# Performance work log

Hardware: AMD Instinct MI355X
Metric: run time of the kernel (lower is better)

The kernel has to match this reference:

```python
import jax, jax.numpy as jnp
import numpy as np

B, S, L, D, M = 32, 256, 64, 100, 20  # batch, n_sentences, max_sentence_len, embed_dim, n_memories


def setup_inputs() -> dict:
    key = jax.random.key(0)
    ks = jax.random.split(key, 6)
    batch = jax.random.normal(ks[0], (B, S, L, D), dtype=jnp.float32)
    enc_mult = jnp.ones((L, D), dtype=jnp.float32)  # input_encoder_multiplier (init to ones)
    keys = 0.1 * jax.random.normal(ks[1], (M, D), dtype=jnp.float32)
    U = 0.1 * jax.random.normal(ks[2], (D, D), dtype=jnp.float32)  # nn.Linear weight [out,in]
    V = 0.1 * jax.random.normal(ks[3], (D, D), dtype=jnp.float32)
    W = 0.1 * jax.random.normal(ks[4], (D, D), dtype=jnp.float32)
    prelu_a = jnp.ones((), dtype=jnp.float32)  # PReLU(init=1), single shared parameter
    return {"batch": batch, "enc_mult": enc_mult, "keys": keys, "U": U, "V": V, "W": W, "prelu_a": prelu_a}


def reference(batch, enc_mult, keys, U, V, W, prelu_a):
    # Encode: elementwise multiply by learned positional multiplier, sum over words -> [B, S, D]
    enc = (batch * enc_mult).sum(axis=2)

    def prelu(x):
        return jnp.where(x >= 0, x, prelu_a * x)

    # keys @ V.T is step-invariant
    keysV = jnp.einsum('md,ed->me', keys, V)  # [M, D]

    def step(mem, s):  # mem: [B, M, D], s: [B, D]
        memory_gate = jnp.einsum('bd,bmd->bm', s, mem)          # [B, M]
        key_gate = jnp.einsum('bd,md->bm', s, keys)              # [B, M]
        gate = jax.nn.sigmoid(memory_gate + key_gate)            # [B, M]
        cand = prelu(
            jnp.einsum('bmd,ed->bme', mem, U)                    # U(memories)
            + keysV[None, :, :]                                  # V(keys)
            + jnp.einsum('bd,ed->be', s, W)[:, None, :]          # W(sentence), broadcast over M
        )
        mem = mem + cand * gate[:, :, None]
        mem = mem / jnp.linalg.norm(mem, axis=2, keepdims=True)  # L2 normalize each memory slot
        return mem, None

    mem0 = jnp.broadcast_to(keys[None, :, :], (B, M, D))  # memories init = keys repeated per batch
    mem_final, _ = jax.lax.scan(step, mem0, jnp.swapaxes(enc, 0, 1))  # scan over sentences
    return mem_final
```

## Files before the change

### kernel.cpp

```cpp
#include <hip/hip_runtime.h>


typedef float v2f __attribute__((ext_vector_type(2)));

__global__ __launch_bounds__(320) void encode_k(
    const float* __restrict__ batch,
    const float* __restrict__ encm,
    float* __restrict__ enc)
{
    __shared__ float prod[6400];
    __shared__ float part[200];
    const int t = threadIdx.x;
    const int row = blockIdx.x;
    const float4* rb = (const float4*)batch + (size_t)row * 1600;
    const float4* e4 = (const float4*)encm;
    float4* p4 = (float4*)prod;
    #pragma unroll
    for (int i = 0; i < 5; ++i) {
        const int idx = i * 320 + t;
        float4 x = rb[idx];
        float4 mu = e4[idx];
        float4 p;
        p.x = x.x * mu.x; p.y = x.y * mu.y; p.z = x.z * mu.z; p.w = x.w * mu.w;
        p4[idx] = p;
    }
    __syncthreads();
    if (t < 200) {
        const int c = (t < 100) ? t : (t - 100);
        const int l0 = (t < 100) ? 0 : 32;
        float s0 = 0.f, s1 = 0.f;
        #pragma unroll
        for (int l = 0; l < 32; l += 2) {
            s0 += prod[(l0 + l) * 100 + c];
            s1 += prod[(l0 + l + 1) * 100 + c];
        }
        part[t] = s0 + s1;
    }
    __syncthreads();
    if (t < 100) enc[(size_t)row * 100 + t] = part[t] + part[100 + t];
}

__global__ void prep_k(const float* __restrict__ W,
                       const float* __restrict__ keys,
                       float* __restrict__ T)
{
    const int d = blockIdx.x;
    const int e = threadIdx.x;
    float v = 0.f;
    if (e < 100) v = W[e * 100 + d];
    else if (e < 120) v = keys[(e - 100) * 100 + d];
    T[d * 128 + e] = v;
}

__global__ __launch_bounds__(128) void project_k(
    const float* __restrict__ enc,
    const float* __restrict__ T,
    float* __restrict__ sWp,
    float* __restrict__ kg)
{
    __shared__ float encS[400];
    const int t = threadIdx.x;
    const int row0 = blockIdx.x * 4;
    if (t < 100) ((float4*)encS)[t] = ((const float4*)(enc + (size_t)row0 * 100))[t];
    __syncthreads();
    float a0 = 0.f, a1 = 0.f, a2 = 0.f, a3 = 0.f;
    #pragma unroll 4
    for (int d = 0; d < 100; ++d) {
        const float w = T[d * 128 + t];
        a0 += w * encS[d];
        a1 += w * encS[100 + d];
        a2 += w * encS[200 + d];
        a3 += w * encS[300 + d];
    }
    if (t < 100) {
        sWp[(size_t)row0 * 100 + t]       = a0;
        sWp[(size_t)(row0 + 1) * 100 + t] = a1;
        sWp[(size_t)(row0 + 2) * 100 + t] = a2;
        sWp[(size_t)(row0 + 3) * 100 + t] = a3;
    } else if (t < 120) {
        const int m = t - 100;
        kg[(size_t)row0 * 20 + m]       = a0;
        kg[(size_t)(row0 + 1) * 20 + m] = a1;
        kg[(size_t)(row0 + 2) * 20 + m] = a2;
        kg[(size_t)(row0 + 3) * 20 + m] = a3;
    }
}

template <int CTRL>
__device__ __forceinline__ float dpp_add_f(float x) {
    int s = __builtin_amdgcn_update_dpp(0, __float_as_int(x), CTRL, 0xF, 0xF, true);
    return x + __int_as_float(s);
}
#define DPP6(v) v = dpp_add_f<0x111>(v); v = dpp_add_f<0x112>(v); v = dpp_add_f<0x114>(v); \
                v = dpp_add_f<0x118>(v); v = dpp_add_f<0x142>(v); v = dpp_add_f<0x143>(v);

#define MATVEC(QOUT, CBPTR)                                             \
    {                                                                   \
        v2f A0 = {0.f,0.f}, A1 = {0.f,0.f};                             \
        v2f A2 = {0.f,0.f}, A3 = {0.f,0.f};                             \
        _Pragma("unroll")                                               \
        for (int j = 0; j < 25; ++j) {                                  \
            float4 cc = (CBPTR)[j];                                     \
            v2f lo = {cc.x, cc.y}, hi4 = {cc.z, cc.w};                  \
            if (j & 1) {                                                \
                A2 = __builtin_elementwise_fma(UE[2*j],   lo,  A2);     \
                A3 = __builtin_elementwise_fma(UE[2*j+1], hi4, A3);     \
            } else {                                                    \
                A0 = __builtin_elementwise_fma(UE[2*j],   lo,  A0);     \
                A1 = __builtin_elementwise_fma(UE[2*j+1], hi4, A1);     \
            }                                                           \
        }                                                               \
        v2f S = (A0 + A1) + (A2 + A3);                                  \
        QOUT = S.x + S.y;                                               \
    }

__global__ __launch_bounds__(128) void entnet_scan(
    const float* __restrict__ enc,
    const float* __restrict__ sWp,
    const float* __restrict__ kg,
    const float* __restrict__ keys,
    const float* __restrict__ U,
    const float* __restrict__ V,
    const float* __restrict__ paPtr,
    float* __restrict__ out)
{
    __shared__ float4 cbuf4[2][32];
    __shared__ float4 red[2][2];
    float* cbuf = (float*)cbuf4;
    const int tid  = threadIdx.x;
    const int lane = tid & 63;
    const int wid  = tid >> 6;
    const int xcd = blockIdx.x & 7;
    const int gg  = blockIdx.x >> 3;
    const int b = xcd * 4 + gg / 20;
    const int m = gg % 20;
    const bool act = (tid < 100);
    const float h = act ? 1.f : 0.f;
    const int e = act ? tid : 99;
    const float pa = paPtr[0];

    v2f UE[50];
    {
        const float4* u = (const float4*)(U + e * 100);
        #pragma unroll
        for (int k = 0; k < 25; ++k) {
            float4 a = u[k];
            UE[2*k]   = (v2f){a.x, a.y};
            UE[2*k+1] = (v2f){a.z, a.w};
        }
    }

    float kv = 0.f;
    {
        const float4* km = (const float4*)(keys + m * 100);
        const float4* vv = (const float4*)(V + e * 100);
        #pragma unroll
        for (int k = 0; k < 25; ++k) {
            float4 a = vv[k], kk = km[k];
            kv += a.x * kk.x + a.y * kk.y + a.z * kk.z + a.w * kk.w;
        }
    }

    const float* encRow = enc + (size_t)b * 25600;
    const float* sWRow  = sWp + (size_t)b * 25600;
    const float* kgRow  = kg + (size_t)b * 5120 + m;

    const float k0 = keys[m * 100 + e];
    float nm = k0;

    cbuf[128 + tid] = k0;
    float nq  = h * k0 * k0;
    const float sv0 = encRow[e];
    float q1i = h * sv0 * k0;
    DPP6(nq) DPP6(q1i)
    if (lane == 63) red[1][wid] = (float4){nq, q1i, 0.f, 0.f};
    __syncthreads();

    float P;
    {
        const float4* cb1 = (const float4*)(&cbuf[128]);
        MATVEC(P, cb1);
    }
    float nsq, g;
    {
        float4 r0 = red[1][0], r1 = red[1][1];
        nsq = r0.x + r1.x;
        const float Q1 = r0.y + r1.y;
        g = 1.f / (1.f + __expf(-(Q1 + kgRow[0])));
    }
    float rn = 1.f;
    float sw = sWRow[e];

    for (int step = 0; step < 256; ++step) {
        const int nxt = (step < 255 ? step + 1 : 255);
        const float nsv = encRow[nxt * 100 + e];
        const float nsw = sWRow[nxt * 100 + e];
        const float nkg = kgRow[nxt * 20];

        const float x = rn * P + kv + sw;
        const float c = (x >= 0.f) ? x : pa * x;
        const int bi = step & 1;
        cbuf[bi * 128 + tid] = c;

        float q3  = h * nm * c;
        float p4  = h * c * c;
        float q0  = h * nsv * nm;
        float r1v = h * nsv * c;
        #define RND4(C) q3 = dpp_add_f<C>(q3); p4 = dpp_add_f<C>(p4); \
                        q0 = dpp_add_f<C>(q0); r1v = dpp_add_f<C>(r1v);
        RND4(0x111) RND4(0x112) RND4(0x114) RND4(0x118) RND4(0x142) RND4(0x143)
        #undef RND4
        if (lane == 63) red[bi][wid] = (float4){q3, p4, q0, r1v};
        __syncthreads();

        float Q;
        {
            const float4* cb = (const float4*)(&cbuf[bi * 128]);
            MATVEC(Q, cb);
        }

        float4 ra = red[bi][0], rb = red[bi][1];
        const float Q3 = ra.x + rb.x;
        const float P4 = ra.y + rb.y;
        const float Q0 = ra.z + rb.z;
        const float R1 = ra.w + rb.w;

        const float n2  = nsq + 2.f * (g * rn) * Q3 + g * g * P4;
        const float rnn = rsqrtf(n2);
        nsq = 1.f;

        nm = rn * nm + g * c;
        P  = rn * P  + g * Q;

        const float Q1 = rn * Q0 + g * R1;
        g = 1.f / (1.f + __expf(-(rnn * Q1 + nkg)));

        rn = rnn;
        sw = nsw;
    }
    if (act) out[(size_t)(b * 20 + m) * 100 + tid] = nm * rn;
}

extern "C" void kernel_launch(void* const* d_in, const int* in_sizes, int n_in,
                              void* d_out, int out_size, void* d_ws, size_t ws_size,
                              hipStream_t stream) {
    const float* batch = (const float*)d_in[0];
    const float* encm  = (const float*)d_in[1];
    const float* keys  = (const float*)d_in[2];
    const float* U     = (const float*)d_in[3];
    const float* V     = (const float*)d_in[4];
    const float* W     = (const float*)d_in[5];
    const float* pa    = (const float*)d_in[6];
    float* out = (float*)d_out;

    float* enc = (float*)d_ws;
    float* sWp = enc + 819200;
    float* kgb = sWp + 819200;
    float* T   = kgb + 163840;

    encode_k<<<8192, 320, 0, stream>>>(batch, encm, enc);
    prep_k<<<100, 128, 0, stream>>>(W, keys, T);
    project_k<<<2048, 128, 0, stream>>>(enc, T, sWp, kgb);
    entnet_scan<<<640, 128, 0, stream>>>(enc, sWp, kgb, keys, U, V, pa, out);
}
```

Measured before the change: 531.0 us.

## Process two memory slots per block in the scan kernel

Each scan block now advances two memory slots (m and m+10) of the same batch element instead of one, halving the grid from 640 to 320 blocks. The U row held in registers is reused for two matvecs per step, and the shared sentence/W loads and barrier are amortized over both slots. This also doubles the independent instruction streams per step, which can hide latency on the serial 256-step chain. The cost is more registers per thread, longer per-step work, and half as many blocks spread across the CUs.

```diff
diff --git a/kernel.cpp b/kernel.cpp
--- a/kernel.cpp
+++ b/kernel.cpp
@@ -94,24 +94,32 @@
 #define DPP6(v) v = dpp_add_f<0x111>(v); v = dpp_add_f<0x112>(v); v = dpp_add_f<0x114>(v); \
                 v = dpp_add_f<0x118>(v); v = dpp_add_f<0x142>(v); v = dpp_add_f<0x143>(v);
 
-#define MATVEC(QOUT, CBPTR)                                             \
+#define MATVEC2(QA_, QB_, CA4, CB4)                                     \
     {                                                                   \
-        v2f A0 = {0.f,0.f}, A1 = {0.f,0.f};                             \
-        v2f A2 = {0.f,0.f}, A3 = {0.f,0.f};                             \
+        v2f A0 = {0.f,0.f}, A1 = {0.f,0.f}, A2 = {0.f,0.f}, A3 = {0.f,0.f}; \
+        v2f B0 = {0.f,0.f}, B1 = {0.f,0.f}, B2 = {0.f,0.f}, B3 = {0.f,0.f}; \
         _Pragma("unroll")                                               \
         for (int j = 0; j < 25; ++j) {                                  \
-            float4 cc = (CBPTR)[j];                                     \
-            v2f lo = {cc.x, cc.y}, hi4 = {cc.z, cc.w};                  \
+            float4 ca = (CA4)[j];                                       \
+            float4 cb = (CB4)[j];                                       \
+            v2f alo = {ca.x, ca.y}, ahi = {ca.z, ca.w};                 \
+            v2f blo = {cb.x, cb.y}, bhi = {cb.z, cb.w};                 \
             if (j & 1) {                                                \
-                A2 = __builtin_elementwise_fma(UE[2*j],   lo,  A2);     \
-                A3 = __builtin_elementwise_fma(UE[2*j+1], hi4, A3);     \
+                A2 = __builtin_elementwise_fma(UE[2*j],   alo, A2);     \
+                A3 = __builtin_elementwise_fma(UE[2*j+1], ahi, A3);     \
+                B2 = __builtin_elementwise_fma(UE[2*j],   blo, B2);     \
+                B3 = __builtin_elementwise_fma(UE[2*j+1], bhi, B3);     \
             } else {                                                    \
-                A0 = __builtin_elementwise_fma(UE[2*j],   lo,  A0);     \
-                A1 = __builtin_elementwise_fma(UE[2*j+1], hi4, A1);     \
+                A0 = __builtin_elementwise_fma(UE[2*j],   alo, A0);     \
+                A1 = __builtin_elementwise_fma(UE[2*j+1], ahi, A1);     \
+                B0 = __builtin_elementwise_fma(UE[2*j],   blo, B0);     \
+                B1 = __builtin_elementwise_fma(UE[2*j+1], bhi, B1);     \
             }                                                           \
         }                                                               \
-        v2f S = (A0 + A1) + (A2 + A3);                                  \
-        QOUT = S.x + S.y;                                               \
+        v2f SA = (A0 + A1) + (A2 + A3);                                 \
+        v2f SB = (B0 + B1) + (B2 + B3);                                 \
+        QA_ = SA.x + SA.y;                                              \
+        QB_ = SB.x + SB.y;                                              \
     }
 
 __global__ __launch_bounds__(128) void entnet_scan(
@@ -124,16 +132,16 @@
     const float* __restrict__ paPtr,
     float* __restrict__ out)
 {
-    __shared__ float4 cbuf4[2][32];
-    __shared__ float4 red[2][2];
-    float* cbuf = (float*)cbuf4;
+    __shared__ float cbuf[2][2][128];
+    __shared__ float4 red[2][2][2];
     const int tid  = threadIdx.x;
     const int lane = tid & 63;
     const int wid  = tid >> 6;
     const int xcd = blockIdx.x & 7;
     const int gg  = blockIdx.x >> 3;
-    const int b = xcd * 4 + gg / 20;
-    const int m = gg % 20;
+    const int b  = xcd * 4 + gg / 10;
+    const int mA = gg % 10;
+    const int mB = mA + 10;
     const bool act = (tid < 100);
     const float h = act ? 1.f : 0.f;
     const int e = act ? tid : 99;
@@ -150,95 +158,122 @@
         }
     }
 
-    float kv = 0.f;
+    float kvA = 0.f, kvB = 0.f;
     {
-        const float4* km = (const float4*)(keys + m * 100);
+        const float4* kmA = (const float4*)(keys + mA * 100);
+        const float4* kmB = (const float4*)(keys + mB * 100);
         const float4* vv = (const float4*)(V + e * 100);
         #pragma unroll
         for (int k = 0; k < 25; ++k) {
-            float4 a = vv[k], kk = km[k];
-            kv += a.x * kk.x + a.y * kk.y + a.z * kk.z + a.w * kk.w;
+            float4 a = vv[k], ka = kmA[k], kb = kmB[k];
+            kvA += a.x * ka.x + a.y * ka.y + a.z * ka.z + a.w * ka.w;
+            kvB += a.x * kb.x + a.y * kb.y + a.z * kb.z + a.w * kb.w;
         }
     }
 
     const float* encRow = enc + (size_t)b * 25600;
     const float* sWRow  = sWp + (size_t)b * 25600;
-    const float* kgRow  = kg + (size_t)b * 5120 + m;
-
-    const float k0 = keys[m * 100 + e];
-    float nm = k0;
-
-    cbuf[128 + tid] = k0;
-    float nq  = h * k0 * k0;
+    const float* kgRowA = kg + (size_t)b * 5120 + mA;
+    const float* kgRowB = kg + (size_t)b * 5120 + mB;
+
+    const float k0A = keys[mA * 100 + e];
+    const float k0B = keys[mB * 100 + e];
+    float nmA = k0A, nmB = k0B;
+
+    cbuf[1][0][tid] = k0A;
+    cbuf[1][1][tid] = k0B;
     const float sv0 = encRow[e];
-    float q1i = h * sv0 * k0;
-    DPP6(nq) DPP6(q1i)
-    if (lane == 63) red[1][wid] = (float4){nq, q1i, 0.f, 0.f};
+    float nqA  = h * k0A * k0A;
+    float nqB  = h * k0B * k0B;
+    float q1iA = h * sv0 * k0A;
+    float q1iB = h * sv0 * k0B;
+    #define RNDI(C) nqA = dpp_add_f<C>(nqA); nqB = dpp_add_f<C>(nqB); \
+                    q1iA = dpp_add_f<C>(q1iA); q1iB = dpp_add_f<C>(q1iB);
+    RNDI(0x111) RNDI(0x112) RNDI(0x114) RNDI(0x118) RNDI(0x142) RNDI(0x143)
+    #undef RNDI
+    if (lane == 63) {
+        red[1][0][wid] = (float4){nqA, q1iA, 0.f, 0.f};
+        red[1][1][wid] = (float4){nqB, q1iB, 0.f, 0.f};
+    }
     __syncthreads();
 
-    float P;
+    float PA, PB;
+    MATVEC2(PA, PB, (const float4*)&cbuf[1][0][0], (const float4*)&cbuf[1][1][0]);
+
+    float nsqA, nsqB, gA, gB;
     {
-        const float4* cb1 = (const float4*)(&cbuf[128]);
-        MATVEC(P, cb1);
-    }
-    float nsq, g;
-    {
-        float4 r0 = red[1][0], r1 = red[1][1];
-        nsq = r0.x + r1.x;
-        const float Q1 = r0.y + r1.y;
-        g = 1.f / (1.f + __expf(-(Q1 + kgRow[0])));
-    }
-    float rn = 1.f;
+        float4 a0 = red[1][0][0], a1 = red[1][0][1];
+        float4 b0 = red[1][1][0], b1 = red[1][1][1];
+        nsqA = a0.x + a1.x;
+        nsqB = b0.x + b1.x;
+        gA = 1.f / (1.f + __expf(-((a0.y + a1.y) + kgRowA[0])));
+        gB = 1.f / (1.f + __expf(-((b0.y + b1.y) + kgRowB[0])));
+    }
+    float rnA = 1.f, rnB = 1.f;
     float sw = sWRow[e];
 
     for (int step = 0; step < 256; ++step) {
         const int nxt = (step < 255 ? step + 1 : 255);
         const float nsv = encRow[nxt * 100 + e];
         const float nsw = sWRow[nxt * 100 + e];
-        const float nkg = kgRow[nxt * 20];
-
-        const float x = rn * P + kv + sw;
-        const float c = (x >= 0.f) ? x : pa * x;
+        const float nkgA = kgRowA[nxt * 20];
+        const float nkgB = kgRowB[nxt * 20];
+
+        const float xA = rnA * PA + kvA + sw;
+        const float xB = rnB * PB + kvB + sw;
+        const float cA = h * ((xA >= 0.f) ? xA : pa * xA);
+        const float cB = h * ((xB >= 0.f) ? xB : pa * xB);
         const int bi = step & 1;
-        cbuf[bi * 128 + tid] = c;
-
-        float q3  = h * nm * c;
-        float p4  = h * c * c;
-        float q0  = h * nsv * nm;
-        float r1v = h * nsv * c;
-        #define RND4(C) q3 = dpp_add_f<C>(q3); p4 = dpp_add_f<C>(p4); \
-                        q0 = dpp_add_f<C>(q0); r1v = dpp_add_f<C>(r1v);
-        RND4(0x111) RND4(0x112) RND4(0x114) RND4(0x118) RND4(0x142) RND4(0x143)
-        #undef RND4
-        if (lane == 63) red[bi][wid] = (float4){q3, p4, q0, r1v};
+        cbuf[bi][0][tid] = cA;
+        cbuf[bi][1][tid] = cB;
+
+        float q3A = nmA * cA, p4A = cA * cA, q0A = h * nsv * nmA, r1A = nsv * cA;
+        float q3B = nmB * cB, p4B = cB * cB, q0B = h * nsv * nmB, r1B = nsv * cB;
+        #define RND8(C) q3A = dpp_add_f<C>(q3A); p4A = dpp_add_f<C>(p4A); \
+                        q0A = dpp_add_f<C>(q0A); r1A = dpp_add_f<C>(r1A); \
+                        q3B = dpp_add_f<C>(q3B); p4B = dpp_add_f<C>(p4B); \
+                        q0B = dpp_add_f<C>(q0B); r1B = dpp_add_f<C>(r1B);
+        RND8(0x111) RND8(0x112) RND8(0x114) RND8(0x118) RND8(0x142) RND8(0x143)
+        #undef RND8
+        if (lane == 63) {
+            red[bi][0][wid] = (float4){q3A, p4A, q0A, r1A};
+            red[bi][1][wid] = (float4){q3B, p4B, q0B, r1B};
+        }
         __syncthreads();
 
-        float Q;
-        {
-            const float4* cb = (const float4*)(&cbuf[bi * 128]);
-            MATVEC(Q, cb);
-        }
-
-        float4 ra = red[bi][0], rb = red[bi][1];
-        const float Q3 = ra.x + rb.x;
-        const float P4 = ra.y + rb.y;
-        const float Q0 = ra.z + rb.z;
-        const float R1 = ra.w + rb.w;
-
-        const float n2  = nsq + 2.f * (g * rn) * Q3 + g * g * P4;
-        const float rnn = rsqrtf(n2);
-        nsq = 1.f;
-
-        nm = rn * nm + g * c;
-        P  = rn * P  + g * Q;
-
-        const float Q1 = rn * Q0 + g * R1;
-        g = 1.f / (1.f + __expf(-(rnn * Q1 + nkg)));
-
-        rn = rnn;
+        float QA, QB;
+        MATVEC2(QA, QB, (const float4*)&cbuf[bi][0][0], (const float4*)&cbuf[bi][1][0]);
+
+        float4 ra0 = red[bi][0][0], ra1 = red[bi][0][1];
+        float4 rb0 = red[bi][1][0], rb1 = red[bi][1][1];
+        const float Q3A = ra0.x + ra1.x, P4A = ra0.y + ra1.y;
+        const float Q0A = ra0.z + ra1.z, R1A = ra0.w + ra1.w;
+        const float Q3B = rb0.x + rb1.x, P4B = rb0.y + rb1.y;
+        const float Q0B = rb0.z + rb1.z, R1B = rb0.w + rb1.w;
+
+        const float n2A = nsqA + 2.f * (gA * rnA) * Q3A + gA * gA * P4A;
+        const float n2B = nsqB + 2.f * (gB * rnB) * Q3B + gB * gB * P4B;
+        const float rnnA = rsqrtf(n2A);
+        const float rnnB = rsqrtf(n2B);
+        nsqA = 1.f; nsqB = 1.f;
+
+        nmA = rnA * nmA + gA * cA;
+        nmB = rnB * nmB + gB * cB;
+        PA  = rnA * PA  + gA * QA;
+        PB  = rnB * PB  + gB * QB;
+
+        const float Q1A = rnA * Q0A + gA * R1A;
+        const float Q1B = rnB * Q0B + gB * R1B;
+        gA = 1.f / (1.f + __expf(-(rnnA * Q1A + nkgA)));
+        gB = 1.f / (1.f + __expf(-(rnnB * Q1B + nkgB)));
+
+        rnA = rnnA; rnB = rnnB;
         sw = nsw;
     }
-    if (act) out[(size_t)(b * 20 + m) * 100 + tid] = nm * rn;
+    if (act) {
+        out[(size_t)(b * 20 + mA) * 100 + tid] = nmA * rnA;
+        out[(size_t)(b * 20 + mB) * 100 + tid] = nmB * rnB;
+    }
 }
 
 extern "C" void kernel_launch(void* const* d_in, const int* in_sizes, int n_in,
@@ -261,5 +296,5 @@
     encode_k<<<8192, 320, 0, stream>>>(batch, encm, enc);
     prep_k<<<100, 128, 0, stream>>>(W, keys, T);
     project_k<<<2048, 128, 0, stream>>>(enc, T, sWp, kgb);
-    entnet_scan<<<640, 128, 0, stream>>>(enc, sWp, kgb, keys, U, V, pa, out);
-}
+    entnet_scan<<<320, 128, 0, stream>>>(enc, sWp, kgb, keys, U, V, pa, out);
+}
```

New measurement: 684.5 us. 1.29x slower.
